# Performance work log

Measured on AMD Instinct MI355X. Metric: run time of the kernel, lower is better.

## Reference

```python
import jax, jax.numpy as jnp
import numpy as np

NUM_HEADS = 12
NUM_PATCHES = 196


def _make_relative_distance_index(num_patches=NUM_PATCHES):
    size = int(np.sqrt(num_patches))  # 14
    coords = np.stack(np.meshgrid(np.arange(size), np.arange(size), indexing='ij'))  # [2,14,14]
    flat = coords.reshape(2, -1)  # [2,196]
    rel = flat[:, None, :] - flat[:, :, None]  # [2,196,196]
    rel = rel.transpose(1, 2, 0).astype(np.int64)  # [196,196,2]
    rel[:, :, 0] += size - 1
    rel[:, :, 1] += size - 1
    rel[:, :, 0] *= 2 * size - 1
    idx = rel.sum(-1) + 1  # shift for cls slot at table row 0
    full = np.zeros((num_patches + 1, num_patches + 1), dtype=np.int64)
    full[1:, 1:] = idx
    return full


def setup_inputs() -> dict:
    key = jax.random.key(0)
    k1, k2, k3, k4, k5 = jax.random.split(key, 5)
    B, N, C = 64, NUM_PATCHES + 1, 768
    table_size = (2 * int(np.sqrt(NUM_PATCHES)) - 1) ** 2 + 1  # 730
    x = jax.random.normal(k1, (B, N, C), dtype=jnp.float32)
    table = jax.random.normal(k2, (table_size, NUM_HEADS), dtype=jnp.float32) * 0.02
    w_qkv = jax.random.normal(k3, (3 * C, C), dtype=jnp.float32) * 0.02
    w_proj = jax.random.normal(k4, (C, C), dtype=jnp.float32) * 0.02
    b_proj = jax.random.normal(k5, (C,), dtype=jnp.float32) * 0.02
    rel_index = jnp.asarray(_make_relative_distance_index())
    return {"x": x, "table": table, "w_qkv": w_qkv, "w_proj": w_proj,
            "b_proj": b_proj, "rel_index": rel_index}


def reference(x, table, w_qkv, w_proj, b_proj, rel_index):
    B, N, C = x.shape
    H = NUM_HEADS
    hd = C // H
    scale = hd ** -0.5
    # qkv projection: [B,N,3C] -> [3,B,H,N,hd]
    qkv = (x @ w_qkv.T).reshape(B, N, 3, H, hd).transpose(2, 0, 3, 1, 4)
    q, k, v = qkv[0], qkv[1], qkv[2]
    # gathered relative position bias: [N,N,H] -> [H,N,N]
    bias = table[rel_index].transpose(2, 0, 1)
    scores = jnp.einsum('bhnd,bhmd->bhnm', q, k) * scale + bias[None]
    attn = jax.nn.softmax(scores, axis=-1)
    out = jnp.einsum('bhnm,bhmd->bhnd', attn, v)
    out = out.transpose(0, 2, 1, 3).reshape(B, N, C)
    return out @ w_proj.T + b_proj
```

## Files before the change

### kernel.cpp

```cpp
#include <hip/hip_runtime.h>


#define NB   64
#define NN   197
#define NC   768
#define NH   12
#define HD   64
#define MM   (NB*NN)
#define MR   12672
#define NP   208
#define SZQ  ((size_t)NB * NH * NN * HD)

typedef unsigned short ushort_t;
typedef __attribute__((ext_vector_type(8))) short short8;
typedef __attribute__((ext_vector_type(4))) float f32x4;
union U128 { uint4 u; short8 s; };

__device__ __forceinline__ unsigned bf16_rne(float f) {
    unsigned u = __float_as_uint(f);
    return (u + 0x7fffu + ((u >> 16) & 1u)) >> 16;
}

__device__ __forceinline__ void gld16(unsigned short* lds, const unsigned short* g) {
    __builtin_amdgcn_global_load_lds(
        (const __attribute__((address_space(1))) void*)g,
        (__attribute__((address_space(3))) void*)lds, 16, 0, 0);
}

__global__ __launch_bounds__(256) void convert_all(
    const float* __restrict__ x, const float* __restrict__ w_qkv,
    const float* __restrict__ w_proj,
    ushort_t* __restrict__ xh, ushort_t* __restrict__ wh,
    ushort_t* __restrict__ wp)
{
    int idx = blockIdx.x * 256 + threadIdx.x;
    if (idx >= (MM + 2304 + 768) * 192) return;
    int r = idx / 192;
    int c = (idx - r * 192) * 4;
    const float* src;
    ushort_t* dsth;
    if (r < MM) {
        src = x + (size_t)r * NC; dsth = xh + (size_t)r * NC + c;
    } else if (r < MM + 2304) {
        int rr = r - MM;
        src = w_qkv + (size_t)rr * NC; dsth = wh + (size_t)rr * NC + c;
    } else {
        int rr = r - MM - 2304;
        src = w_proj + (size_t)rr * NC; dsth = wp + (size_t)rr * NC + c;
    }
    float4 f = *(const float4*)(src + c);
    ushort4 hv = { (ushort_t)bf16_rne(f.x), (ushort_t)bf16_rne(f.y),
                   (ushort_t)bf16_rne(f.z), (ushort_t)bf16_rne(f.w) };
    *(ushort4*)dsth = hv;
}

__global__ __launch_bounds__(256) void bias_precompute(
    const float* __restrict__ table, const int* __restrict__ rel_index,
    float* __restrict__ biasP)
{
    int i = blockIdx.x * 256 + threadIdx.x;
    if (i >= NH * 13 * 13 * 256) return;
    int r = i & 3, l15 = (i >> 2) & 15, quad = (i >> 6) & 3;
    int t = i >> 8;
    int kt = t % 13; int t2 = t / 13;
    int qt = t2 % 13; int h = t2 / 13;
    int n = qt * 16 + quad * 4 + r;
    int m = kt * 16 + l15;
    float v = -1e30f;
    if (n < NN && m < NN) v = table[rel_index[n * NN + m] * NH + h];
    biasP[i] = v;
}

__device__ __forceinline__ void gemm_mainloop(
    const ushort_t* __restrict__ A2, int sA,
    const ushort_t* __restrict__ B2, int sB,
    int m0, int n0, int kiters, ushort_t* Abuf, ushort_t* Bbuf, f32x4 acc[4][4])
{
    const int tid = threadIdx.x;
    const int w = tid >> 6, lane = tid & 63;
    const int wm = w & 1, wn = w >> 1;
    const int lr = lane >> 3, lc = lane & 7;
    const int gch = lc ^ lr;

    const ushort_t* Ag = A2 + (size_t)(m0 + w * 32 + lr) * sA + gch * 8;
    const ushort_t* Bg = B2 + (size_t)(n0 + w * 32 + lr) * sB + gch * 8;
    ushort_t* Al = Abuf + (w * 32) * 64;
    ushort_t* Bl = Bbuf + (w * 32) * 64;

    int aoff[4], boff[4];
    const int quad = lane >> 4, l15 = lane & 15;
    #pragma unroll
    for (int t = 0; t < 4; t++) {
        int ra = wm * 64 + t * 16 + l15;
        aoff[t] = ra * 64 + ((quad ^ (ra & 7)) << 3);
        int rb = wn * 64 + t * 16 + l15;
        boff[t] = rb * 64 + ((quad ^ (rb & 7)) << 3);
    }

    for (int ks = 0; ks < kiters; ks++) {
        __syncthreads();
        #pragma unroll
        for (int it = 0; it < 4; it++) {
            gld16(Al + it * 8 * 64, Ag + (size_t)it * 8 * sA);
            gld16(Bl + it * 8 * 64, Bg + (size_t)it * 8 * sB);
        }
        __syncthreads();
        #pragma unroll
        for (int k0 = 0; k0 < 2; k0++) {
            U128 af[4], bf[4];
            #pragma unroll
            for (int t = 0; t < 4; t++) {
                af[t].u = *(const uint4*)&Abuf[aoff[t] ^ (k0 << 5)];
                bf[t].u = *(const uint4*)&Bbuf[boff[t] ^ (k0 << 5)];
            }
            #pragma unroll
            for (int i = 0; i < 4; i++)
                #pragma unroll
                for (int j = 0; j < 4; j++)
                    acc[i][j] = __builtin_amdgcn_mfma_f32_16x16x32_bf16(
                        af[i].s, bf[j].s, acc[i][j], 0, 0, 0);
        }
        Ag += 64; Bg += 64;
    }
}

__global__ __launch_bounds__(256) void gemm_qkv_mfma(
    const ushort_t* __restrict__ A2, const ushort_t* __restrict__ B2,
    ushort_t* __restrict__ qbf, ushort_t* __restrict__ kbf,
    ushort_t* __restrict__ vbf)
{
    __shared__ ushort_t Abuf[128 * 64];
    __shared__ ushort_t Bbuf[128 * 64];
    f32x4 acc[4][4];
    f32x4 z = {0.f, 0.f, 0.f, 0.f};
    #pragma unroll
    for (int i = 0; i < 4; i++)
        #pragma unroll
        for (int j = 0; j < 4; j++) acc[i][j] = z;

    const int m0 = blockIdx.y * 128, n0 = blockIdx.x * 128;
    gemm_mainloop(A2, NC, B2, NC, m0, n0, 12, Abuf, Bbuf, acc);

    const int tid = threadIdx.x;
    const int w = tid >> 6, lane = tid & 63;
    const int wm = w & 1, wn = w >> 1;
    const int quad = lane >> 4, l15 = lane & 15;

    size_t baseo[4][4];
    bool valid[4][4];
    #pragma unroll
    for (int mt = 0; mt < 4; mt++) {
        #pragma unroll
        for (int r = 0; r < 4; r++) {
            int m = m0 + wm * 64 + mt * 16 + quad * 4 + r;
            valid[mt][r] = (m < MM);
            int mc = valid[mt][r] ? m : 0;
            int b_ = mc / NN, n_ = mc - b_ * NN;
            baseo[mt][r] = ((size_t)b_ * NH * NN + n_) * HD;
        }
    }
    #pragma unroll
    for (int nt = 0; nt < 4; nt++) {
        int c0 = n0 + wn * 64 + nt * 16;
        int tq = c0 / NC;
        int wi = c0 - tq * NC;
        int hh = wi >> 6;
        int d0 = (wi & 63) + l15;
        ushort_t* dst = (tq == 0) ? qbf : (tq == 1) ? kbf : vbf;
        float scale = (tq == 0) ? 0.125f : 1.0f;
        size_t hoff = (size_t)hh * (NN * HD) + d0;
        #pragma unroll
        for (int mt = 0; mt < 4; mt++) {
            #pragma unroll
            for (int r = 0; r < 4; r++) {
                if (valid[mt][r])
                    dst[baseo[mt][r] + hoff] = (ushort_t)bf16_rne(acc[mt][nt][r] * scale);
            }
        }
    }
}

__global__ __launch_bounds__(256) void gemm_proj_mfma(
    const ushort_t* __restrict__ A2, const ushort_t* __restrict__ B2,
    const float* __restrict__ bias, float* __restrict__ out)
{
    __shared__ ushort_t Abuf[128 * 64];
    __shared__ ushort_t Bbuf[128 * 64];
    f32x4 acc[4][4];
    f32x4 z = {0.f, 0.f, 0.f, 0.f};
    #pragma unroll
    for (int i = 0; i < 4; i++)
        #pragma unroll
        for (int j = 0; j < 4; j++) acc[i][j] = z;

    const int m0 = blockIdx.y * 128, n0 = blockIdx.x * 128;
    gemm_mainloop(A2, NC, B2, NC, m0, n0, 12, Abuf, Bbuf, acc);

    const int tid = threadIdx.x;
    const int w = tid >> 6, lane = tid & 63;
    const int wm = w & 1, wn = w >> 1;
    const int quad = lane >> 4, l15 = lane & 15;
    #pragma unroll
    for (int nt = 0; nt < 4; nt++) {
        int col = n0 + wn * 64 + nt * 16 + l15;
        float bi = bias[col];
        #pragma unroll
        for (int mt = 0; mt < 4; mt++) {
            #pragma unroll
            for (int r = 0; r < 4; r++) {
                int m = m0 + wm * 64 + mt * 16 + quad * 4 + r;
                if (m < MM)
                    out[(size_t)m * NC + col] = acc[mt][nt][r] + bi;
            }
        }
    }
}

__global__ __launch_bounds__(256) void attn_mfma(
    const ushort_t* __restrict__ qbf, const ushort_t* __restrict__ kbf,
    const ushort_t* __restrict__ vbf, const float* __restrict__ biasP,
    ushort_t* __restrict__ ab)
{
    __shared__ ushort_t Vt[64 * 232];
    __shared__ ushort_t Pl[4][16 * 232];

    const int bh = blockIdx.x;
    const int b = bh / NH, h = bh % NH;
    const int tid = threadIdx.x;
    const int w = tid >> 6, lane = tid & 63;
    const int quad = lane >> 4, l15 = lane & 15;
    const size_t base = (size_t)bh * (NN * HD);
    const ushort_t* kg = kbf + base;
    const ushort_t* vg = vbf + base;
    const ushort_t* qg = qbf + base;

    ushort_t* Vstage = &Pl[0][0];
    for (int idx = tid; idx < NP * 8; idx += 256) {
        int row = idx >> 3, ch = idx & 7;
        uint4 val = {0u, 0u, 0u, 0u};
        if (row < NN) val = *(const uint4*)(vg + (size_t)row * HD + ch * 8);
        *(uint4*)&Vstage[row * HD + ch * 8] = val;
    }
    __syncthreads();
    for (int task = tid; task < 64 * 29; task += 256) {
        int d = task & 63, kc = task >> 6;
        ushort_t tmp[8];
        #pragma unroll
        for (int j = 0; j < 8; j++) {
            int key = kc * 8 + j;
            tmp[j] = (key < NP) ? Vstage[key * HD + d] : (ushort_t)0;
        }
        uint4 u;
        u.x = (unsigned)tmp[0] | ((unsigned)tmp[1] << 16);
        u.y = (unsigned)tmp[2] | ((unsigned)tmp[3] << 16);
        u.z = (unsigned)tmp[4] | ((unsigned)tmp[5] << 16);
        u.w = (unsigned)tmp[6] | ((unsigned)tmp[7] << 16);
        *(uint4*)&Vt[d * 232 + kc * 8] = u;
    }
    __syncthreads();

    const int worker = blockIdx.y * 4 + w;

    #pragma unroll
    for (int rep = 0; rep < 2; rep++) {
        int qt = worker + rep * 8;
        if (qt > 12) break;
        const int q0 = qt * 16;

        int qrow = q0 + l15; if (qrow > NN - 1) qrow = NN - 1;
        U128 qf0, qf1;
        qf0.u = *(const uint4*)(qg + (size_t)qrow * HD + quad * 8);
        qf1.u = *(const uint4*)(qg + (size_t)qrow * HD + 32 + quad * 8);

        f32x4 S[13];
        const float* bp = biasP + ((size_t)(h * 13 + qt) * 13) * 256 + (quad << 6) + (l15 << 2);
        #pragma unroll
        for (int kt = 0; kt < 13; kt++) {
            float4 bv = *(const float4*)(bp + kt * 256);
            S[kt][0] = bv.x; S[kt][1] = bv.y; S[kt][2] = bv.z; S[kt][3] = bv.w;
        }

        #pragma unroll
        for (int kt = 0; kt < 13; kt++) {
            int krow = kt * 16 + l15; if (krow > NN - 1) krow = NN - 1;
            U128 k0, k1;
            k0.u = *(const uint4*)(kg + (size_t)krow * HD + quad * 8);
            k1.u = *(const uint4*)(kg + (size_t)krow * HD + 32 + quad * 8);
            S[kt] = __builtin_amdgcn_mfma_f32_16x16x32_bf16(qf0.s, k0.s, S[kt], 0, 0, 0);
            S[kt] = __builtin_amdgcn_mfma_f32_16x16x32_bf16(qf1.s, k1.s, S[kt], 0, 0, 0);
        }

        ushort_t* P = Pl[w];
        #pragma unroll
        for (int r = 0; r < 4; r++) {
            float mx = S[0][r];
            #pragma unroll
            for (int kt = 1; kt < 13; kt++) mx = fmaxf(mx, S[kt][r]);
            mx = fmaxf(mx, __shfl_xor(mx, 1));
            mx = fmaxf(mx, __shfl_xor(mx, 2));
            mx = fmaxf(mx, __shfl_xor(mx, 4));
            mx = fmaxf(mx, __shfl_xor(mx, 8));
            float sum = 0.f;
            #pragma unroll
            for (int kt = 0; kt < 13; kt++) {
                float e = __expf(S[kt][r] - mx);
                S[kt][r] = e;
                sum += e;
            }
            sum += __shfl_xor(sum, 1);
            sum += __shfl_xor(sum, 2);
            sum += __shfl_xor(sum, 4);
            sum += __shfl_xor(sum, 8);
            float inv = 1.0f / sum;
            int prow = quad * 4 + r;
            #pragma unroll
            for (int kt = 0; kt < 13; kt++)
                P[prow * 232 + kt * 16 + l15] = (ushort_t)bf16_rne(S[kt][r] * inv);
        }
        #pragma unroll
        for (int z = 0; z < 3; z++) {
            int idx = z * 64 + lane;
            int row = idx / 12, c = idx - row * 12;
            *(unsigned*)&P[row * 232 + NP + 2 * c] = 0u;
        }

        f32x4 O[4];
        f32x4 z4 = {0.f, 0.f, 0.f, 0.f};
        #pragma unroll
        for (int dt = 0; dt < 4; dt++) O[dt] = z4;
        #pragma unroll
        for (int ks = 0; ks < 7; ks++) {
            U128 pf;
            pf.u = *(const uint4*)&P[l15 * 232 + ks * 32 + quad * 8];
            #pragma unroll
            for (int dt = 0; dt < 4; dt++) {
                U128 vf;
                vf.u = *(const uint4*)&Vt[(dt * 16 + l15) * 232 + ks * 32 + quad * 8];
                O[dt] = __builtin_amdgcn_mfma_f32_16x16x32_bf16(pf.s, vf.s, O[dt], 0, 0, 0);
            }
        }

        float* Osh = (float*)&Pl[w][0];
        #pragma unroll
        for (int dt = 0; dt < 4; dt++)
            #pragma unroll
            for (int r = 0; r < 4; r++)
                Osh[(quad * 4 + r) * 68 + dt * 16 + l15] = O[dt][r];
        int orow = lane >> 2;
        int d0 = (lane & 3) << 4;
        int q = q0 + orow;
        if (q < NN) {
            unsigned hiw[8];
            #pragma unroll
            for (int k4 = 0; k4 < 4; k4++) {
                float4 f = *(const float4*)&Osh[orow * 68 + d0 + k4 * 4];
                unsigned h0 = bf16_rne(f.x), h1 = bf16_rne(f.y);
                unsigned h2 = bf16_rne(f.z), h3 = bf16_rne(f.w);
                hiw[k4 * 2]     = h0 | (h1 << 16);
                hiw[k4 * 2 + 1] = h2 | (h3 << 16);
            }
            size_t baseo = ((size_t)b * NN + q) * NC + h * HD + d0;
            uint4 hA = {hiw[0], hiw[1], hiw[2], hiw[3]};
            uint4 hB = {hiw[4], hiw[5], hiw[6], hiw[7]};
            *(uint4*)&ab[baseo] = hA;
            *(uint4*)&ab[baseo + 8] = hB;
        }
    }
}

extern "C" void kernel_launch(void* const* d_in, const int* in_sizes, int n_in,
                              void* d_out, int out_size, void* d_ws, size_t ws_size,
                              hipStream_t stream)
{
    const float* x        = (const float*)d_in[0];
    const float* table    = (const float*)d_in[1];
    const float* w_qkv    = (const float*)d_in[2];
    const float* w_proj   = (const float*)d_in[3];
    const float* b_proj   = (const float*)d_in[4];
    const int*   rel_idx  = (const int*)d_in[5];
    float* out = (float*)d_out;

    ushort_t* xh  = (ushort_t*)d_ws;
    ushort_t* wh  = xh + (size_t)MR * NC;
    ushort_t* wp  = wh + (size_t)2304 * NC;
    ushort_t* ab  = wp + (size_t)768 * NC;
    ushort_t* qbf = ab + (size_t)MR * NC;
    ushort_t* kbf = qbf + SZQ;
    ushort_t* vbf = kbf + SZQ;
    float* biasP  = (float*)(vbf + SZQ);

    const int cvt_quads = (MM + 2304 + 768) * 192;
    convert_all<<<(cvt_quads + 255) / 256, 256, 0, stream>>>(
        x, w_qkv, w_proj, xh, wh, wp);
    bias_precompute<<<(NH * 13 * 13 * 256 + 255) / 256, 256, 0, stream>>>(
        table, rel_idx, biasP);

    gemm_qkv_mfma<<<dim3(18, 99), 256, 0, stream>>>(xh, wh, qbf, kbf, vbf);
    attn_mfma<<<dim3(NB * NH, 2), 256, 0, stream>>>(qbf, kbf, vbf, biasP, ab);
    gemm_proj_mfma<<<dim3(6, 99), 256, 0, stream>>>(ab, wp, b_proj, out);
}
```

Baseline: 280.5 us.

## Use 256x256 double-buffered GEMM tiles with 512 threads and XCD-aware block mapping

```diff
diff --git a/kernel.cpp b/kernel.cpp
--- a/kernel.cpp
+++ b/kernel.cpp
@@ -7,7 +7,7 @@
 #define NH   12
 #define HD   64
 #define MM   (NB*NN)
-#define MR   12672
+#define MR   12800
 #define NP   208
 #define SZQ  ((size_t)NB * NH * NN * HD)
 
@@ -26,6 +26,10 @@
         (const __attribute__((address_space(1))) void*)g,
         (__attribute__((address_space(3))) void*)lds, 16, 0, 0);
 }
+
+#define BAR() do { asm volatile("" ::: "memory"); \
+                   __builtin_amdgcn_s_barrier();  \
+                   asm volatile("" ::: "memory"); } while (0)
 
 __global__ __launch_bounds__(256) void convert_all(
     const float* __restrict__ x, const float* __restrict__ w_qkv,
@@ -71,146 +75,206 @@
     biasP[i] = v;
 }
 
-__device__ __forceinline__ void gemm_mainloop(
+__device__ __forceinline__ void gemm256_loop(
     const ushort_t* __restrict__ A2, int sA,
     const ushort_t* __restrict__ B2, int sB,
-    int m0, int n0, int kiters, ushort_t* Abuf, ushort_t* Bbuf, f32x4 acc[4][4])
+    int m0, int n0, int kiters,
+    ushort_t* Abuf, ushort_t* Bbuf, f32x4 (&acc)[8][4])
 {
     const int tid = threadIdx.x;
     const int w = tid >> 6, lane = tid & 63;
     const int wm = w & 1, wn = w >> 1;
     const int lr = lane >> 3, lc = lane & 7;
     const int gch = lc ^ lr;
+    const int quad = lane >> 4, l15 = lane & 15;
 
     const ushort_t* Ag = A2 + (size_t)(m0 + w * 32 + lr) * sA + gch * 8;
     const ushort_t* Bg = B2 + (size_t)(n0 + w * 32 + lr) * sB + gch * 8;
-    ushort_t* Al = Abuf + (w * 32) * 64;
-    ushort_t* Bl = Bbuf + (w * 32) * 64;
-
-    int aoff[4], boff[4];
-    const int quad = lane >> 4, l15 = lane & 15;
-    #pragma unroll
-    for (int t = 0; t < 4; t++) {
-        int ra = wm * 64 + t * 16 + l15;
-        aoff[t] = ra * 64 + ((quad ^ (ra & 7)) << 3);
-        int rb = wn * 64 + t * 16 + l15;
-        boff[t] = rb * 64 + ((quad ^ (rb & 7)) << 3);
-    }
-
-    for (int ks = 0; ks < kiters; ks++) {
-        __syncthreads();
-        #pragma unroll
-        for (int it = 0; it < 4; it++) {
-            gld16(Al + it * 8 * 64, Ag + (size_t)it * 8 * sA);
-            gld16(Bl + it * 8 * 64, Bg + (size_t)it * 8 * sB);
-        }
-        __syncthreads();
-        #pragma unroll
-        for (int k0 = 0; k0 < 2; k0++) {
-            U128 af[4], bf[4];
-            #pragma unroll
-            for (int t = 0; t < 4; t++) {
-                af[t].u = *(const uint4*)&Abuf[aoff[t] ^ (k0 << 5)];
-                bf[t].u = *(const uint4*)&Bbuf[boff[t] ^ (k0 << 5)];
-            }
-            #pragma unroll
-            for (int i = 0; i < 4; i++)
-                #pragma unroll
-                for (int j = 0; j < 4; j++)
-                    acc[i][j] = __builtin_amdgcn_mfma_f32_16x16x32_bf16(
-                        af[i].s, bf[j].s, acc[i][j], 0, 0, 0);
-        }
-        Ag += 64; Bg += 64;
-    }
-}
-
-__global__ __launch_bounds__(256) void gemm_qkv_mfma(
+
+    const int sw = (quad ^ (l15 & 7)) << 3;
+    int aoff[8], boff[4];
+    #pragma unroll
+    for (int i = 0; i < 8; i++) aoff[i] = (wm * 128 + i * 16 + l15) * 64 + sw;
+    #pragma unroll
+    for (int j = 0; j < 4; j++) boff[j] = (wn * 64 + j * 16 + l15) * 64 + sw;
+
+    {
+        ushort_t* Al = Abuf + (w * 32) * 64;
+        ushort_t* Bl = Bbuf + (w * 32) * 64;
+        #pragma unroll
+        for (int c = 0; c < 4; c++) {
+            gld16(Al + c * 8 * 64, Ag + (size_t)c * 8 * sA);
+            gld16(Bl + c * 8 * 64, Bg + (size_t)c * 8 * sB);
+        }
+    }
+
+    #define MFMA16(I0) do { \
+        __builtin_amdgcn_s_setprio(1); \
+        _Pragma("unroll") \
+        for (int i_ = 0; i_ < 4; i_++) \
+            _Pragma("unroll") \
+            for (int j_ = 0; j_ < 4; j_++) \
+                acc[(I0) + i_][j_] = __builtin_amdgcn_mfma_f32_16x16x32_bf16( \
+                    af[i_].s, bf[j_].s, acc[(I0) + i_][j_], 0, 0, 0); \
+        __builtin_amdgcn_s_setprio(0); } while (0)
+
+    for (int t = 0; t < kiters; ++t) {
+        const int cur = t & 1;
+        const ushort_t* Ac = Abuf + cur * 16384;
+        const ushort_t* Bc = Bbuf + cur * 16384;
+        ushort_t* An = Abuf + (cur ^ 1) * 16384 + (w * 32) * 64;
+        ushort_t* Bn = Bbuf + (cur ^ 1) * 16384 + (w * 32) * 64;
+        const ushort_t* AgN = Ag + (size_t)(t + 1) * 64;
+        const ushort_t* BgN = Bg + (size_t)(t + 1) * 64;
+        const bool pf = (t + 1 < kiters);
+
+        if (pf) {
+            gld16(An, AgN);
+            gld16(Bn, BgN);
+            asm volatile("s_waitcnt vmcnt(2)" ::: "memory");
+        } else {
+            asm volatile("s_waitcnt vmcnt(0)" ::: "memory");
+        }
+        BAR();
+
+        U128 af[4], bf[4];
+        #pragma unroll
+        for (int j = 0; j < 4; j++) bf[j].u = *(const uint4*)&Bc[boff[j]];
+        #pragma unroll
+        for (int i = 0; i < 4; i++) af[i].u = *(const uint4*)&Ac[aoff[i]];
+        if (pf) { gld16(An + 8 * 64, AgN + (size_t)8 * sA);
+                  gld16(Bn + 8 * 64, BgN + (size_t)8 * sB); }
+        BAR();
+        MFMA16(0);
+
+        #pragma unroll
+        for (int i = 0; i < 4; i++) af[i].u = *(const uint4*)&Ac[aoff[4 + i]];
+        if (pf) { gld16(An + 16 * 64, AgN + (size_t)16 * sA);
+                  gld16(Bn + 16 * 64, BgN + (size_t)16 * sB); }
+        BAR();
+        MFMA16(4);
+
+        #pragma unroll
+        for (int j = 0; j < 4; j++) bf[j].u = *(const uint4*)&Bc[boff[j] ^ 32];
+        #pragma unroll
+        for (int i = 0; i < 4; i++) af[i].u = *(const uint4*)&Ac[aoff[i] ^ 32];
+        if (pf) { gld16(An + 24 * 64, AgN + (size_t)24 * sA);
+                  gld16(Bn + 24 * 64, BgN + (size_t)24 * sB); }
+        BAR();
+        MFMA16(0);
+
+        #pragma unroll
+        for (int i = 0; i < 4; i++) af[i].u = *(const uint4*)&Ac[aoff[4 + i] ^ 32];
+        BAR();
+        MFMA16(4);
+
+        BAR();
+    }
+    #undef MFMA16
+}
+
+__global__ __launch_bounds__(512) void gemm_qkv_mfma(
     const ushort_t* __restrict__ A2, const ushort_t* __restrict__ B2,
     ushort_t* __restrict__ qbf, ushort_t* __restrict__ kbf,
     ushort_t* __restrict__ vbf)
 {
-    __shared__ ushort_t Abuf[128 * 64];
-    __shared__ ushort_t Bbuf[128 * 64];
-    f32x4 acc[4][4];
+    __shared__ ushort_t Abuf[2 * 16384];
+    __shared__ ushort_t Bbuf[2 * 16384];
+    f32x4 acc[8][4];
     f32x4 z = {0.f, 0.f, 0.f, 0.f};
     #pragma unroll
-    for (int i = 0; i < 4; i++)
+    for (int i = 0; i < 8; i++)
         #pragma unroll
         for (int j = 0; j < 4; j++) acc[i][j] = z;
 
-    const int m0 = blockIdx.y * 128, n0 = blockIdx.x * 128;
-    gemm_mainloop(A2, NC, B2, NC, m0, n0, 12, Abuf, Bbuf, acc);
+    const int NWG = 450, NTN = 9;
+    int bid = blockIdx.x;
+    int q8 = NWG >> 3, r8 = NWG & 7;
+    int xcd = bid & 7, loc = bid >> 3;
+    int nid = (xcd < r8 ? xcd * (q8 + 1) : r8 * (q8 + 1) + (xcd - r8) * q8) + loc;
+    int mt = nid / NTN, nt = nid - mt * NTN;
+    const int m0 = mt * 256, n0 = nt * 256;
+
+    gemm256_loop(A2, NC, B2, NC, m0, n0, 12, Abuf, Bbuf, acc);
 
     const int tid = threadIdx.x;
     const int w = tid >> 6, lane = tid & 63;
     const int wm = w & 1, wn = w >> 1;
     const int quad = lane >> 4, l15 = lane & 15;
 
-    size_t baseo[4][4];
-    bool valid[4][4];
-    #pragma unroll
-    for (int mt = 0; mt < 4; mt++) {
+    int mbase[8][4];
+    bool mval[8][4];
+    #pragma unroll
+    for (int i = 0; i < 8; i++) {
         #pragma unroll
         for (int r = 0; r < 4; r++) {
-            int m = m0 + wm * 64 + mt * 16 + quad * 4 + r;
-            valid[mt][r] = (m < MM);
-            int mc = valid[mt][r] ? m : 0;
+            int m = m0 + wm * 128 + i * 16 + quad * 4 + r;
+            mval[i][r] = (m < MM);
+            int mc = mval[i][r] ? m : 0;
             int b_ = mc / NN, n_ = mc - b_ * NN;
-            baseo[mt][r] = ((size_t)b_ * NH * NN + n_) * HD;
-        }
-    }
-    #pragma unroll
-    for (int nt = 0; nt < 4; nt++) {
-        int c0 = n0 + wn * 64 + nt * 16;
+            mbase[i][r] = b_ * NH * NN + n_;
+        }
+    }
+    #pragma unroll
+    for (int j = 0; j < 4; j++) {
+        int c0 = n0 + wn * 64 + j * 16;
         int tq = c0 / NC;
         int wi = c0 - tq * NC;
         int hh = wi >> 6;
         int d0 = (wi & 63) + l15;
         ushort_t* dst = (tq == 0) ? qbf : (tq == 1) ? kbf : vbf;
         float scale = (tq == 0) ? 0.125f : 1.0f;
-        size_t hoff = (size_t)hh * (NN * HD) + d0;
-        #pragma unroll
-        for (int mt = 0; mt < 4; mt++) {
+        int hoff = hh * (NN * HD) + d0;
+        #pragma unroll
+        for (int i = 0; i < 8; i++) {
             #pragma unroll
             for (int r = 0; r < 4; r++) {
-                if (valid[mt][r])
-                    dst[baseo[mt][r] + hoff] = (ushort_t)bf16_rne(acc[mt][nt][r] * scale);
+                if (mval[i][r])
+                    dst[(size_t)mbase[i][r] * HD + hoff] =
+                        (ushort_t)bf16_rne(acc[i][j][r] * scale);
             }
         }
     }
 }
 
-__global__ __launch_bounds__(256) void gemm_proj_mfma(
+__global__ __launch_bounds__(512) void gemm_proj_mfma(
     const ushort_t* __restrict__ A2, const ushort_t* __restrict__ B2,
     const float* __restrict__ bias, float* __restrict__ out)
 {
-    __shared__ ushort_t Abuf[128 * 64];
-    __shared__ ushort_t Bbuf[128 * 64];
-    f32x4 acc[4][4];
+    __shared__ ushort_t Abuf[2 * 16384];
+    __shared__ ushort_t Bbuf[2 * 16384];
+    f32x4 acc[8][4];
     f32x4 z = {0.f, 0.f, 0.f, 0.f};
     #pragma unroll
-    for (int i = 0; i < 4; i++)
+    for (int i = 0; i < 8; i++)
         #pragma unroll
         for (int j = 0; j < 4; j++) acc[i][j] = z;
 
-    const int m0 = blockIdx.y * 128, n0 = blockIdx.x * 128;
-    gemm_mainloop(A2, NC, B2, NC, m0, n0, 12, Abuf, Bbuf, acc);
+    const int NWG = 150, NTN = 3;
+    int bid = blockIdx.x;
+    int q8 = NWG >> 3, r8 = NWG & 7;
+    int xcd = bid & 7, loc = bid >> 3;
+    int nid = (xcd < r8 ? xcd * (q8 + 1) : r8 * (q8 + 1) + (xcd - r8) * q8) + loc;
+    int mt = nid / NTN, nt = nid - mt * NTN;
+    const int m0 = mt * 256, n0 = nt * 256;
+
+    gemm256_loop(A2, NC, B2, NC, m0, n0, 12, Abuf, Bbuf, acc);
 
     const int tid = threadIdx.x;
     const int w = tid >> 6, lane = tid & 63;
     const int wm = w & 1, wn = w >> 1;
     const int quad = lane >> 4, l15 = lane & 15;
     #pragma unroll
-    for (int nt = 0; nt < 4; nt++) {
-        int col = n0 + wn * 64 + nt * 16 + l15;
+    for (int j = 0; j < 4; j++) {
+        int col = n0 + wn * 64 + j * 16 + l15;
         float bi = bias[col];
         #pragma unroll
-        for (int mt = 0; mt < 4; mt++) {
+        for (int i = 0; i < 8; i++) {
             #pragma unroll
             for (int r = 0; r < 4; r++) {
-                int m = m0 + wm * 64 + mt * 16 + quad * 4 + r;
+                int m = m0 + wm * 128 + i * 16 + quad * 4 + r;
                 if (m < MM)
-                    out[(size_t)m * NC + col] = acc[mt][nt][r] + bi;
+                    out[(size_t)m * NC + col] = acc[i][j][r] + bi;
             }
         }
     }
@@ -395,7 +459,7 @@
     bias_precompute<<<(NH * 13 * 13 * 256 + 255) / 256, 256, 0, stream>>>(
         table, rel_idx, biasP);
 
-    gemm_qkv_mfma<<<dim3(18, 99), 256, 0, stream>>>(xh, wh, qbf, kbf, vbf);
+    gemm_qkv_mfma<<<450, 512, 0, stream>>>(xh, wh, qbf, kbf, vbf);
     attn_mfma<<<dim3(NB * NH, 2), 256, 0, stream>>>(qbf, kbf, vbf, biasP, ab);
-    gemm_proj_mfma<<<dim3(6, 99), 256, 0, stream>>>(ab, wp, b_proj, out);
-}
+    gemm_proj_mfma<<<150, 512, 0, stream>>>(ab, wp, b_proj, out);
+}
```

After: 295.7 us. +5.4%, slower.
